# Optimization experiments

Hardware: AMD Instinct MI355X
Metric: run time of the kernel (lower is better)

Reference implementation:

```python
import jax, jax.numpy as jnp
import numpy as np

GROUPS = 8
MAX_DISP = 24
EPS = 1e-5


def group_norm(x, gamma, beta, groups):
    B, C = x.shape[0], x.shape[1]
    spatial = x.shape[2:]
    xg = x.reshape(B, groups, C // groups, -1)
    mean = xg.mean(axis=(2, 3), keepdims=True)
    var = xg.var(axis=(2, 3), keepdims=True)
    xn = ((xg - mean) * jax.lax.rsqrt(var + EPS)).reshape(B, C, *spatial)
    shp = (1, C) + (1,) * len(spatial)
    return xn * gamma.reshape(shp) + beta.reshape(shp)


def conv3d(x, w):
    return jax.lax.conv_general_dilated(x, w, (1, 1, 1), [(1, 1)] * 3,
                                        dimension_numbers=("NCDHW", "OIDHW", "NCDHW"))


def conv2d(x, w):
    return jax.lax.conv_general_dilated(x, w, (1, 1), [(1, 1)] * 2,
                                        dimension_numbers=("NCHW", "OIHW", "NCHW"))


def conv1d(x, w):
    return jax.lax.conv_general_dilated(x, w, (1,), [(1, 1)],
                                        dimension_numbers=("NCW", "OIW", "NCW"))


def setup_inputs() -> dict:
    key = jax.random.key(0)
    ks = jax.random.split(key, 12)
    B, C, H, W = 2, 64, 160, 320
    feat_out = 16
    fL = jax.random.normal(ks[0], (B, C, H, W), dtype=jnp.float32)
    fR = jax.random.normal(ks[1], (B, C, H, W), dtype=jnp.float32)
    def w(k, shape):
        fan_in = int(np.prod(shape[1:]))
        return jax.random.normal(k, shape, dtype=jnp.float32) / np.sqrt(fan_in)
    return {
        "fL": fL, "fR": fR,
        # agg: Conv3d(groups->16) GN SiLU, Conv3d(16->16) GN SiLU, Conv3d(16->1)+bias
        "agg_w1": w(ks[2], (16, GROUPS, 3, 3, 3)),
        "agg_g1": jnp.ones((16,), jnp.float32), "agg_b1": jnp.zeros((16,), jnp.float32),
        "agg_w2": w(ks[3], (16, 16, 3, 3, 3)),
        "agg_g2": jnp.ones((16,), jnp.float32), "agg_b2": jnp.zeros((16,), jnp.float32),
        "agg_w3": w(ks[4], (1, 16, 3, 3, 3)), "agg_bias3": jnp.zeros((1,), jnp.float32),
        # feat_head: Conv2d(C->feat_out) GN SiLU
        "feat_w": w(ks[5], (feat_out, C, 3, 3)),
        "feat_g": jnp.ones((feat_out,), jnp.float32), "feat_b": jnp.zeros((feat_out,), jnp.float32),
        # apc_d: Conv1d(max_disp->max_disp, k=3, no bias)
        "apc_w": w(ks[6], (MAX_DISP, MAX_DISP, 3)),
        "reg_w1": w(ks[7], (32, MAX_DISP + feat_out, 3, 3)),
        "reg_g1": jnp.ones((32,), jnp.float32), "reg_b1": jnp.zeros((32,), jnp.float32),
        "reg_w2": w(ks[8], (1, 32, 3, 3)), "reg_bias2": jnp.zeros((1,), jnp.float32),
    }


def reference(fL, fR, agg_w1, agg_g1, agg_b1, agg_w2, agg_g2, agg_b2,
              agg_w3, agg_bias3, feat_w, feat_g, feat_b, apc_w,
              reg_w1, reg_g1, reg_b1, reg_w2, reg_bias2):
    B, C, H, W = fL.shape
    G, D = GROUPS, MAX_DISP
    cg = C // G
    fL_g = fL.reshape(B, G, cg, H, W)

    # Cost volume: group-wise correlation with right feature shifted by d (zeros on left)
    def corr(d):
        fR_s = fR if d == 0 else jnp.pad(fR, ((0, 0), (0, 0), (0, 0), (d, 0)))[..., :W]
        return (fL_g * fR_s.reshape(B, G, cg, H, W)).mean(axis=2)  # [B,G,H,W]
    cv = jnp.stack([corr(d) for d in range(D)], axis=2)  # [B,G,D,H,W]

    # 3D aggregation
    h = jax.nn.silu(group_norm(conv3d(cv, agg_w1), agg_g1, agg_b1, 8))
    h = jax.nn.silu(group_norm(conv3d(h, agg_w2), agg_g2, agg_b2, 8))
    logits = (conv3d(h, agg_w3) + agg_bias3.reshape(1, 1, 1, 1, 1)).squeeze(1)  # [B,D,H,W]

    # Soft-argmin
    prob = jax.nn.softmax(logits, axis=1)
    disp_idx = jnp.arange(D, dtype=logits.dtype).reshape(1, D, 1, 1)
    d_sa = (prob * disp_idx).sum(axis=1, keepdims=True)  # [B,1,H,W]
    conf = prob.max(axis=1, keepdims=True)

    feat = jax.nn.silu(group_norm(conv2d(fL, feat_w), feat_g, feat_b, 8))  # [B,16,H,W]

    apc_out = conv1d(logits.reshape(B, D, H * W), apc_w).reshape(B, D, H, W)
    head_in = jnp.concatenate([apc_out, feat], axis=1)
    h2 = jax.nn.silu(group_norm(conv2d(head_in, reg_w1), reg_g1, reg_b1, 8))
    delta = conv2d(h2, reg_w2) + reg_bias2.reshape(1, 1, 1, 1)
    d_init = d_sa + delta

    sx = jnp.zeros_like(d_init)
    sy = jnp.zeros_like(d_init)
    return (d_init, sx, sy, feat, conf)
```

## Files before the change

### kernel.cpp

```cpp
#include <hip/hip_runtime.h>
#include <hip/hip_bf16.h>
#include <math.h>

constexpr int B_ = 2;
constexpr int C_ = 64;
constexpr int H_ = 160;
constexpr int W_ = 320;
constexpr int G_ = 8;
constexpr int D_ = 24;
constexpr int HW_ = H_ * W_;
constexpr int DHW_ = D_ * HW_;
constexpr float EPS_ = 1e-5f;

typedef __bf16 b8 __attribute__((ext_vector_type(8)));
typedef float  f4 __attribute__((ext_vector_type(4)));

__device__ inline float bf_lo(unsigned u) { return __builtin_bit_cast(float, u << 16); }
__device__ inline float bf_hi(unsigned u) { return __builtin_bit_cast(float, u & 0xffff0000u); }
__device__ inline unsigned pack2(float a, float b) {
  unsigned lo = __builtin_bit_cast(unsigned short, (__bf16)a);
  unsigned hi = __builtin_bit_cast(unsigned short, (__bf16)b);
  return (hi << 16) | lo;
}
__device__ inline float silu(float v) { return v / (1.f + __expf(-v)); }

__global__ __launch_bounds__(320)
void cv_cl_kernel(const float* __restrict__ fL, const float* __restrict__ fR,
                  __bf16* __restrict__ cv) {
  int w = threadIdx.x;
  int h = blockIdx.x % H_;
  int b = blockIdx.x / H_;
  int d0 = blockIdx.y * 6;
  const size_t rowbase = ((size_t)(b * C_) * H_ + h) * W_;
  float l[C_];
#pragma unroll
  for (int c = 0; c < C_; c++) l[c] = fL[rowbase + (size_t)c * HW_ + w];
  for (int dd = 0; dd < 6; dd++) {
    int d = d0 + dd;
    float s[8] = {0.f,0.f,0.f,0.f,0.f,0.f,0.f,0.f};
    if (w >= d) {
      const float* pr = fR + rowbase + (w - d);
#pragma unroll
      for (int c = 0; c < C_; c++) s[c >> 3] += l[c] * pr[(size_t)c * HW_];
    }
    b8 r;
#pragma unroll
    for (int g = 0; g < 8; g++) r[g] = (__bf16)(s[g] * 0.125f);
    *(b8*)(cv + ((size_t)((b * D_ + d) * H_ + h) * W_ + w) * 8) = r;
  }
}

__global__ void wprep_kernel(const float* __restrict__ w1, const float* __restrict__ w2,
                             __bf16* __restrict__ wf1, __bf16* __restrict__ wf2) {
  int lane = threadIdx.x;
  int co = lane & 15, kb = lane >> 4;
#pragma unroll
  for (int p = 0; p < 7; p++)
#pragma unroll
    for (int j = 0; j < 8; j++) {
      int kl = kb * 8 + j;
      int tap = p * 4 + (kl >> 3);
      int ci = kl & 7;
      float v = (tap <= 26) ? w1[(co * 8 + ci) * 27 + tap] : 0.f;
      wf1[(p * 64 + lane) * 8 + j] = (__bf16)v;
    }
#pragma unroll
  for (int p = 0; p < 14; p++)
#pragma unroll
    for (int j = 0; j < 8; j++) {
      int kl = kb * 8 + j;
      int tap = p * 2 + (kl >> 4);
      int ci = kl & 15;
      float v = (tap <= 26) ? w2[(co * 16 + ci) * 27 + tap] : 0.f;
      wf2[(p * 64 + lane) * 8 + j] = (__bf16)v;
    }
}

template <int CIN, int PAIRS>
__global__ __launch_bounds__(320)
void conv3d_mfma_kernel(const __bf16* __restrict__ in, const __bf16* __restrict__ wf,
                        __bf16* __restrict__ out) {
  __shared__ __align__(16) __bf16 li[9 * 162 * CIN];
  const int tid = threadIdx.x;
  int bid = blockIdx.x;
  const int wt = bid & 1; bid >>= 1;
  const int h = bid % H_;
  const int d = (bid / H_) % D_;
  const int b = bid / (H_ * D_);
  const int w0 = wt * 160;
  constexpr int VPE = CIN / 8;
  for (int idx = tid; idx < 1458 * VPE; idx += 320) {
    int entry = idx / VPE, half = idx % VPE;
    int pos = entry % 162;
    int r = entry / 162;
    int hh = r % 3, dd = r / 3;
    int dg = d + dd - 1, hg = h + hh - 1, wg = w0 + pos - 1;
    uint4 v = make_uint4(0, 0, 0, 0);
    if ((unsigned)dg < (unsigned)D_ && (unsigned)hg < (unsigned)H_ && (unsigned)wg < (unsigned)W_)
      v = *(const uint4*)(in + ((size_t)((b * D_ + dg) * H_ + hg) * W_ + wg) * CIN + half * 8);
    *(uint4*)(li + (size_t)entry * CIN + half * 8) = v;
  }
  __syncthreads();
  const int lane = tid & 63;
  const int wid = tid >> 6;
  const int m = lane & 15;
  const int tpp = 32 / CIN;
  const int tapsel = (CIN == 16) ? (lane >> 5) : (lane >> 4);
  const int ci0 = (CIN == 16) ? ((lane >> 1) & 8) : 0;
  b8 wfr[PAIRS];
#pragma unroll
  for (int p = 0; p < PAIRS; p++) wfr[p] = *(const b8*)(wf + (p * 64 + lane) * 8);
  int loff[PAIRS];
#pragma unroll
  for (int p = 0; p < PAIRS; p++) {
    int tap = p * tpp + tapsel;
    if (tap > 26) tap = 26;
    int kd = tap / 9, kh = (tap / 3) % 3, kw = tap % 3;
    loff[p] = ((kd * 3 + kh) * 162 + kw) * CIN + ci0;
  }
  const int rowbase = ((b * D_ + d) * H_ + h) * W_ + w0;
  for (int t = 0; t < 2; t++) {
    const int m0 = (wid * 2 + t) * 16;
    const int lbase = (m0 + m) * CIN;
    f4 acc = {0.f, 0.f, 0.f, 0.f};
#pragma unroll
    for (int p = 0; p < PAIRS; p++) {
      b8 a = *(const b8*)(li + lbase + loff[p]);
      acc = __builtin_amdgcn_mfma_f32_16x16x32_bf16(a, wfr[p], acc, 0, 0, 0);
    }
    const int co = lane & 15;
    const int r0 = (lane >> 4) * 4;
    const int pos0 = rowbase + m0;
#pragma unroll
    for (int r = 0; r < 4; r++)
      out[(size_t)(pos0 + r0 + r) * 16 + co] = (__bf16)acc[r];
  }
}

__global__ __launch_bounds__(256)
void stats_cl_kernel(const __bf16* __restrict__ x, double* __restrict__ st) {
  int b = blockIdx.y;
  float sg[8] = {0,0,0,0,0,0,0,0}, sq[8] = {0,0,0,0,0,0,0,0};
  for (int i = blockIdx.x * 256 + threadIdx.x; i < DHW_; i += gridDim.x * 256) {
    const uint4* p = (const uint4*)(x + ((size_t)b * DHW_ + i) * 16);
    uint4 q0 = p[0], q1 = p[1];
    unsigned us[8] = {q0.x, q0.y, q0.z, q0.w, q1.x, q1.y, q1.z, q1.w};
#pragma unroll
    for (int k = 0; k < 8; k++) {
      float v0 = bf_lo(us[k]), v1 = bf_hi(us[k]);
      sg[k] += v0 + v1;
      sq[k] += v0 * v0 + v1 * v1;
    }
  }
#pragma unroll
  for (int k = 0; k < 8; k++)
    for (int off = 32; off; off >>= 1) {
      sg[k] += __shfl_xor(sg[k], off, 64);
      sq[k] += __shfl_xor(sq[k], off, 64);
    }
  __shared__ float ls[4][16];
  int wid = threadIdx.x >> 6, lane = threadIdx.x & 63;
  if (lane == 0) {
#pragma unroll
    for (int k = 0; k < 8; k++) { ls[wid][k] = sg[k]; ls[wid][8 + k] = sq[k]; }
  }
  __syncthreads();
  if (threadIdx.x < 16) {
    float t = ls[0][threadIdx.x] + ls[1][threadIdx.x] + ls[2][threadIdx.x] + ls[3][threadIdx.x];
    int g = threadIdx.x & 7, which = threadIdx.x >> 3;
    atomicAdd(&st[(size_t)(b * 8 + g) * 2 + which], (double)t);
  }
}

__global__ __launch_bounds__(256)
void norm_cl_kernel(__bf16* __restrict__ x, const double* __restrict__ st,
                    const float* __restrict__ gamma, const float* __restrict__ beta,
                    double invN) {
  int b = blockIdx.y;
  __shared__ float scs[16], shs[16];
  if (threadIdx.x < 16) {
    int c = threadIdx.x, grp = c >> 1;
    double mean = st[(size_t)(b * 8 + grp) * 2] * invN;
    double var = st[(size_t)(b * 8 + grp) * 2 + 1] * invN - mean * mean;
    float sc = gamma[c] * rsqrtf((float)var + EPS_);
    scs[c] = sc;
    shs[c] = beta[c] - (float)mean * sc;
  }
  __syncthreads();
  float sc[16], sh[16];
#pragma unroll
  for (int c = 0; c < 16; c++) { sc[c] = scs[c]; sh[c] = shs[c]; }
  for (int i = blockIdx.x * 256 + threadIdx.x; i < DHW_; i += gridDim.x * 256) {
    uint4* p = (uint4*)(x + ((size_t)b * DHW_ + i) * 16);
    uint4 q0 = p[0], q1 = p[1];
    unsigned us[8] = {q0.x, q0.y, q0.z, q0.w, q1.x, q1.y, q1.z, q1.w};
    unsigned ro[8];
#pragma unroll
    for (int k = 0; k < 8; k++) {
      int c0 = 2 * k;
      float v0 = silu(bf_lo(us[k]) * sc[c0] + sh[c0]);
      float v1 = silu(bf_hi(us[k]) * sc[c0 + 1] + sh[c0 + 1]);
      ro[k] = pack2(v0, v1);
    }
    p[0] = make_uint4(ro[0], ro[1], ro[2], ro[3]);
    p[1] = make_uint4(ro[4], ro[5], ro[6], ro[7]);
  }
}

__global__ __launch_bounds__(256)
void conv3_tile_kernel(const __bf16* __restrict__ a2, const float* __restrict__ wt,
                       const float* __restrict__ bias, float* __restrict__ logits) {
  __shared__ __align__(16) __bf16 li[5 * 6 * 2 * 66 * 8];
  __shared__ float lw[432];
  int bid = blockIdx.x;
  int wtile = bid % 5; bid /= 5;
  int ht = bid % 40; bid /= 40;
  int dt = bid % 8; bid /= 8;
  int b = bid;
  const int d0 = dt * 3, h0 = ht * 4, w0 = wtile * 64;
  for (int i = threadIdx.x; i < 432; i += 256) {
    int tap = i >> 4, ci = i & 15;
    lw[i] = wt[ci * 27 + tap];
  }
  for (int idx = threadIdx.x; idx < 5 * 6 * 66; idx += 256) {
    int pos = idx % 66;
    int r = idx / 66;
    int hh = r % 6, dd = r / 6;
    int d = d0 + dd - 1, h = h0 + hh - 1, w = w0 + pos - 1;
    uint4 v0 = make_uint4(0, 0, 0, 0), v1 = v0;
    if ((unsigned)d < (unsigned)D_ && (unsigned)h < (unsigned)H_ && (unsigned)w < (unsigned)W_) {
      const uint4* p = (const uint4*)(a2 + ((size_t)(((b * D_ + d) * H_ + h) * W_ + w)) * 16);
      v0 = p[0];
      v1 = p[1];
    }
    int vb = ((dd * 6 + hh) * 2) * 66 + pos;
    *(uint4*)(li + (size_t)vb * 8) = v0;
    *(uint4*)(li + (size_t)(vb + 66) * 8) = v1;
  }
  __syncthreads();
  const int ow = threadIdx.x & 63;
  const int oh = threadIdx.x >> 6;
  float acc[3] = {0.f, 0.f, 0.f};
  for (int kd = 0; kd < 3; kd++)
    for (int kh = 0; kh < 3; kh++)
      for (int kw = 0; kw < 3; kw++) {
        const int tap = kd * 9 + kh * 3 + kw;
        const float* wp = lw + tap * 16;
        float wv[16];
#pragma unroll
        for (int c = 0; c < 16; c++) wv[c] = wp[c];
        const int hh = oh + kh;
        const int pos = ow + kw;
#pragma unroll
        for (int od = 0; od < 3; od++) {
          const int dd = od + kd;
          const int vb = ((dd * 6 + hh) * 2) * 66 + pos;
          uint4 q0 = *(const uint4*)(li + (size_t)vb * 8);
          uint4 q1 = *(const uint4*)(li + (size_t)(vb + 66) * 8);
          acc[od] +=
            bf_lo(q0.x) * wv[0]  + bf_hi(q0.x) * wv[1]  + bf_lo(q0.y) * wv[2]  + bf_hi(q0.y) * wv[3] +
            bf_lo(q0.z) * wv[4]  + bf_hi(q0.z) * wv[5]  + bf_lo(q0.w) * wv[6]  + bf_hi(q0.w) * wv[7] +
            bf_lo(q1.x) * wv[8]  + bf_hi(q1.x) * wv[9]  + bf_lo(q1.y) * wv[10] + bf_hi(q1.y) * wv[11] +
            bf_lo(q1.z) * wv[12] + bf_hi(q1.z) * wv[13] + bf_lo(q1.w) * wv[14] + bf_hi(q1.w) * wv[15];
        }
      }
  const float bv = bias[0];
#pragma unroll
  for (int od = 0; od < 3; od++)
    logits[((size_t)(b * D_ + d0 + od) * H_ + (h0 + oh)) * W_ + w0 + ow] = acc[od] + bv;
}

template <int C0, int C1, int COUT, int COT, bool HASBIAS, bool ADD_DSA>
__global__ __launch_bounds__(320)
void conv2d_kernel(const float* __restrict__ in0, const float* __restrict__ in1,
                   const float* __restrict__ wt, const float* __restrict__ bias,
                   const float* __restrict__ dsa, float* __restrict__ out) {
  constexpr int CINT = C0 + C1;
  constexpr int CL = COUT / COT;
  __shared__ float lw[CL * CINT * 9];
  const int co0 = blockIdx.y * CL;
  for (int i = threadIdx.x; i < CL * CINT * 9; i += 320) lw[i] = wt[co0 * CINT * 9 + i];
  __syncthreads();
  int w = threadIdx.x;
  int h = blockIdx.x % H_;
  int b = blockIdx.x / H_;
  float acc[CL];
#pragma unroll
  for (int co = 0; co < CL; co++) acc[co] = 0.f;
  for (int kh = 0; kh < 3; kh++) {
    int hh = h + kh - 1;
    if (hh < 0 || hh >= H_) continue;
    for (int kw = 0; kw < 3; kw++) {
      int ww = w + kw - 1;
      if (ww < 0 || ww >= W_) continue;
#pragma unroll
      for (int ci = 0; ci < C0; ci++) {
        float v = in0[((size_t)(b * C0 + ci)) * HW_ + hh * W_ + ww];
        const float* lwp = lw + (ci * 3 + kh) * 3 + kw;
#pragma unroll
        for (int co = 0; co < CL; co++) acc[co] += v * lwp[co * CINT * 9];
      }
      if (C1 > 0) {
#pragma unroll
        for (int ci = 0; ci < (C1 > 0 ? C1 : 1); ci++) {
          float v = in1[((size_t)(b * C1 + ci)) * HW_ + hh * W_ + ww];
          const float* lwp = lw + ((C0 + ci) * 3 + kh) * 3 + kw;
#pragma unroll
          for (int co = 0; co < CL; co++) acc[co] += v * lwp[co * CINT * 9];
        }
      }
    }
  }
#pragma unroll
  for (int co = 0; co < CL; co++) {
    float r = acc[co];
    if (HASBIAS) r += bias[co0 + co];
    if (ADD_DSA) r += dsa[(size_t)b * HW_ + h * W_ + w];
    out[((size_t)(b * COUT + co0 + co)) * HW_ + h * W_ + w] = r;
  }
}

__global__ __launch_bounds__(256)
void conv1d_kernel(const float* __restrict__ logits, const float* __restrict__ wt,
                   float* __restrict__ out) {
  __shared__ float lw[D_ * D_ * 3];
  for (int i = threadIdx.x; i < D_ * D_ * 3; i += 256) lw[i] = wt[i];
  __syncthreads();
  int idx = blockIdx.x * 256 + threadIdx.x;
  int b = idx / HW_;
  int i = idx % HW_;
  float acc[D_];
#pragma unroll
  for (int o = 0; o < D_; o++) acc[o] = 0.f;
  for (int k = 0; k < 3; k++) {
    int pos = i + k - 1;
    if (pos < 0 || pos >= HW_) continue;
#pragma unroll
    for (int din = 0; din < D_; din++) {
      float v = logits[((size_t)b * D_ + din) * HW_ + pos];
      const float* lwp = lw + din * 3 + k;
#pragma unroll
      for (int o = 0; o < D_; o++) acc[o] += v * lwp[o * D_ * 3];
    }
  }
#pragma unroll
  for (int o = 0; o < D_; o++) out[((size_t)b * D_ + o) * HW_ + i] = acc[o];
}

__global__ __launch_bounds__(256)
void stats_kernel(const float* __restrict__ x, double* __restrict__ stats,
                  int Cc, int chg, size_t per_ch, int nchunk) {
  int tmp = blockIdx.x;
  int chunk = tmp % nchunk; tmp /= nchunk;
  int cig = tmp % chg; tmp /= chg;
  int grp = tmp % 8;
  int b = tmp / 8;
  int c = grp * chg + cig;
  size_t len = per_ch / nchunk;
  const float* p = x + ((size_t)b * Cc + c) * per_ch + (size_t)chunk * len;
  float s = 0.f, s2 = 0.f;
  for (size_t i = threadIdx.x; i < len; i += 256) {
    float v = p[i];
    s += v;
    s2 += v * v;
  }
  __shared__ double ls[256], ls2[256];
  ls[threadIdx.x] = (double)s;
  ls2[threadIdx.x] = (double)s2;
  __syncthreads();
  for (int off = 128; off > 0; off >>= 1) {
    if (threadIdx.x < off) {
      ls[threadIdx.x] += ls[threadIdx.x + off];
      ls2[threadIdx.x] += ls2[threadIdx.x + off];
    }
    __syncthreads();
  }
  if (threadIdx.x == 0) {
    atomicAdd(&stats[(size_t)(b * 8 + grp) * 2], ls[0]);
    atomicAdd(&stats[(size_t)(b * 8 + grp) * 2 + 1], ls2[0]);
  }
}

__global__ __launch_bounds__(256)
void norm_silu_f32o_kernel(const float* __restrict__ x, float* __restrict__ y,
                           const double* __restrict__ stats,
                           const float* __restrict__ gamma, const float* __restrict__ beta,
                           int chg, size_t per_ch, double invN) {
  int c = blockIdx.y;
  int b = blockIdx.z;
  int grp = c / chg;
  double s = stats[(size_t)(b * 8 + grp) * 2];
  double s2 = stats[(size_t)(b * 8 + grp) * 2 + 1];
  double mean_d = s * invN;
  double var_d = s2 * invN - mean_d * mean_d;
  float sc = gamma[c] / sqrtf((float)var_d + EPS_);
  float sh = beta[c] - (float)mean_d * sc;
  size_t base = ((size_t)b * gridDim.y + c) * per_ch;
  size_t chunk = (per_ch + gridDim.x - 1) / gridDim.x;
  size_t start = (size_t)blockIdx.x * chunk;
  size_t end = start + chunk;
  if (end > per_ch) end = per_ch;
  for (size_t i = start + threadIdx.x; i < end; i += 256) {
    float v = x[base + i] * sc + sh;
    y[base + i] = v / (1.f + __expf(-v));
  }
}

__global__ __launch_bounds__(320)
void softmax_kernel(const float* __restrict__ logits, float* __restrict__ dsa,
                    float* __restrict__ conf) {
  int w = threadIdx.x;
  int h = blockIdx.x % H_;
  int b = blockIdx.x / H_;
  size_t base = ((size_t)b * D_) * HW_ + h * W_ + w;
  float v[D_];
  float m = -1e30f;
#pragma unroll
  for (int d = 0; d < D_; d++) {
    v[d] = logits[base + (size_t)d * HW_];
    m = fmaxf(m, v[d]);
  }
  float s = 0.f, wd = 0.f;
#pragma unroll
  for (int d = 0; d < D_; d++) {
    float e = __expf(v[d] - m);
    s += e;
    wd += (float)d * e;
  }
  float inv = 1.f / s;
  dsa[(size_t)b * HW_ + h * W_ + w] = wd * inv;
  conf[(size_t)b * HW_ + h * W_ + w] = inv;
}


extern "C" void kernel_launch(void* const* d_in, const int* in_sizes, int n_in,
                              void* d_out, int out_size, void* d_ws, size_t ws_size,
                              hipStream_t stream) {
  const float* fL = (const float*)d_in[0];
  const float* fR = (const float*)d_in[1];
  const float* agg_w1 = (const float*)d_in[2];
  const float* agg_g1 = (const float*)d_in[3];
  const float* agg_b1 = (const float*)d_in[4];
  const float* agg_w2 = (const float*)d_in[5];
  const float* agg_g2 = (const float*)d_in[6];
  const float* agg_b2 = (const float*)d_in[7];
  const float* agg_w3 = (const float*)d_in[8];
  const float* agg_bias3 = (const float*)d_in[9];
  const float* feat_w = (const float*)d_in[10];
  const float* feat_g = (const float*)d_in[11];
  const float* feat_b = (const float*)d_in[12];
  const float* apc_w = (const float*)d_in[13];
  const float* reg_w1 = (const float*)d_in[14];
  const float* reg_g1 = (const float*)d_in[15];
  const float* reg_b1 = (const float*)d_in[16];
  const float* reg_w2 = (const float*)d_in[17];
  const float* reg_bias2 = (const float*)d_in[18];

  char* wsb = (char*)d_ws;
  constexpr size_t REG = 78643200ull;
  __bf16* a1 = (__bf16*)wsb;
  __bf16* cvb = (__bf16*)(wsb + REG);
  __bf16* a2 = (__bf16*)(wsb + REG);
  float* logits = (float*)wsb;
  float* apc = logits + 2457600;
  float* h2 = apc + 2457600;
  float* dsa = h2 + 3276800;
  float* featraw = dsa + 102400;
  __bf16* wf1 = (__bf16*)(wsb + 2 * REG);
  __bf16* wf2 = wf1 + 3584;
  double* stats = (double*)(wsb + 2 * REG + 21504);

  float* out = (float*)d_out;
  float* out_dinit = out;
  float* out_sx = out + 102400;
  float* out_feat = out + 307200;
  float* out_conf = out + 1945600;

  hipMemsetAsync(stats, 0, 128 * sizeof(double), stream);
  hipMemsetAsync(out_sx, 0, 2 * 102400 * sizeof(float), stream);

  wprep_kernel<<<1, 64, 0, stream>>>(agg_w1, agg_w2, wf1, wf2);

  cv_cl_kernel<<<dim3(B_ * H_, 4), 320, 0, stream>>>(fL, fR, cvb);

  conv3d_mfma_kernel<8, 7><<<B_ * D_ * H_ * 2, 320, 0, stream>>>(cvb, wf1, a1);
  stats_cl_kernel<<<dim3(256, B_), 256, 0, stream>>>(a1, stats + 0);
  norm_cl_kernel<<<dim3(512, B_), 256, 0, stream>>>(a1, stats + 0, agg_g1, agg_b1,
                                                    1.0 / (2.0 * DHW_));

  conv3d_mfma_kernel<16, 14><<<B_ * D_ * H_ * 2, 320, 0, stream>>>(a1, wf2, a2);
  stats_cl_kernel<<<dim3(256, B_), 256, 0, stream>>>(a2, stats + 32);
  norm_cl_kernel<<<dim3(512, B_), 256, 0, stream>>>(a2, stats + 32, agg_g2, agg_b2,
                                                    1.0 / (2.0 * DHW_));

  conv3_tile_kernel<<<3200, 256, 0, stream>>>(a2, agg_w3, agg_bias3, logits);

  softmax_kernel<<<B_ * H_, 320, 0, stream>>>(logits, dsa, out_conf);

  conv2d_kernel<C_, 0, 16, 2, false, false><<<dim3(B_ * H_, 2), 320, 0, stream>>>(
      fL, nullptr, feat_w, nullptr, nullptr, featraw);
  stats_kernel<<<B_ * 8 * 2 * 8, 256, 0, stream>>>(featraw, stats + 64, 16, 2, (size_t)HW_, 8);
  norm_silu_f32o_kernel<<<dim3(50, 16, B_), 256, 0, stream>>>(featraw, out_feat, stats + 64,
                                                              feat_g, feat_b, 2, (size_t)HW_,
                                                              1.0 / (2.0 * HW_));

  conv1d_kernel<<<(B_ * HW_) / 256, 256, 0, stream>>>(logits, apc_w, apc);

  conv2d_kernel<D_, 16, 32, 4, false, false><<<dim3(B_ * H_, 4), 320, 0, stream>>>(
      apc, out_feat, reg_w1, nullptr, nullptr, h2);
  stats_kernel<<<B_ * 8 * 4 * 8, 256, 0, stream>>>(h2, stats + 96, 32, 4, (size_t)HW_, 8);
  norm_silu_f32o_kernel<<<dim3(50, 32, B_), 256, 0, stream>>>(h2, h2, stats + 96, reg_g1, reg_b1,
                                                              4, (size_t)HW_, 1.0 / (4.0 * HW_));

  conv2d_kernel<32, 0, 1, 1, true, true><<<dim3(B_ * H_, 1), 320, 0, stream>>>(
      h2, nullptr, reg_w2, reg_bias2, dsa, out_dinit);
}
```

Baseline: 840.5 us.

## Retile 3D conv into 3x4x64 output blocks to cut halo reloads

Each 3D conv block now computes a 3(d)x4(h)x64(w) output tile instead of a single 160-wide row. The shared-memory tile grows to a 5x6x66 halo region, and each of 4 waves loops over 12 M-tiles. Before, every output row reloaded a 3x3 halo of input rows, roughly 9x read amplification; the new tile brings that down to about 2.6x. The cost is a larger LDS footprint per block, which may reduce occupancy, and the per-block loop becomes longer.

```diff
diff --git a/kernel.cpp b/kernel.cpp
--- a/kernel.cpp
+++ b/kernel.cpp
@@ -77,24 +77,24 @@
 }
 
 template <int CIN, int PAIRS>
-__global__ __launch_bounds__(320)
+__global__ __launch_bounds__(256)
 void conv3d_mfma_kernel(const __bf16* __restrict__ in, const __bf16* __restrict__ wf,
                         __bf16* __restrict__ out) {
-  __shared__ __align__(16) __bf16 li[9 * 162 * CIN];
+  __shared__ __align__(16) __bf16 li[5 * 6 * 66 * CIN];
   const int tid = threadIdx.x;
   int bid = blockIdx.x;
-  const int wt = bid & 1; bid >>= 1;
-  const int h = bid % H_;
-  const int d = (bid / H_) % D_;
-  const int b = bid / (H_ * D_);
-  const int w0 = wt * 160;
+  int wtile = bid % 5; bid /= 5;
+  int ht = bid % 40; bid /= 40;
+  int dt = bid % 8; bid /= 8;
+  const int b = bid;
+  const int d0 = dt * 3, h0 = ht * 4, w0 = wtile * 64;
   constexpr int VPE = CIN / 8;
-  for (int idx = tid; idx < 1458 * VPE; idx += 320) {
+  for (int idx = tid; idx < 1980 * VPE; idx += 256) {
     int entry = idx / VPE, half = idx % VPE;
-    int pos = entry % 162;
-    int r = entry / 162;
-    int hh = r % 3, dd = r / 3;
-    int dg = d + dd - 1, hg = h + hh - 1, wg = w0 + pos - 1;
+    int pos = entry % 66;
+    int r = entry / 66;
+    int hh = r % 6, dd = r / 6;
+    int dg = d0 + dd - 1, hg = h0 + hh - 1, wg = w0 + pos - 1;
     uint4 v = make_uint4(0, 0, 0, 0);
     if ((unsigned)dg < (unsigned)D_ && (unsigned)hg < (unsigned)H_ && (unsigned)wg < (unsigned)W_)
       v = *(const uint4*)(in + ((size_t)((b * D_ + dg) * H_ + hg) * W_ + wg) * CIN + half * 8);
@@ -116,24 +116,27 @@
     int tap = p * tpp + tapsel;
     if (tap > 26) tap = 26;
     int kd = tap / 9, kh = (tap / 3) % 3, kw = tap % 3;
-    loff[p] = ((kd * 3 + kh) * 162 + kw) * CIN + ci0;
-  }
-  const int rowbase = ((b * D_ + d) * H_ + h) * W_ + w0;
-  for (int t = 0; t < 2; t++) {
-    const int m0 = (wid * 2 + t) * 16;
-    const int lbase = (m0 + m) * CIN;
+    loff[p] = ((kd * 6 + kh) * 66 + kw) * CIN + ci0;
+  }
+  const int co = lane & 15;
+  const int r0 = (lane >> 4) * 4;
+#pragma unroll 4
+  for (int t = 0; t < 12; t++) {
+    const int mt = wid * 12 + t;
+    const int od = mt >> 4;
+    const int rem = mt & 15;
+    const int oh = rem >> 2, wq = rem & 3;
+    const int lbase = ((od * 6 + oh) * 66 + wq * 16 + m) * CIN;
     f4 acc = {0.f, 0.f, 0.f, 0.f};
 #pragma unroll
     for (int p = 0; p < PAIRS; p++) {
       b8 a = *(const b8*)(li + lbase + loff[p]);
       acc = __builtin_amdgcn_mfma_f32_16x16x32_bf16(a, wfr[p], acc, 0, 0, 0);
     }
-    const int co = lane & 15;
-    const int r0 = (lane >> 4) * 4;
-    const int pos0 = rowbase + m0;
+    const int wbase = ((b * D_ + d0 + od) * H_ + h0 + oh) * W_ + w0 + wq * 16;
 #pragma unroll
     for (int r = 0; r < 4; r++)
-      out[(size_t)(pos0 + r0 + r) * 16 + co] = (__bf16)acc[r];
+      out[(size_t)(wbase + r0 + r) * 16 + co] = (__bf16)acc[r];
   }
 }
 
@@ -483,12 +486,12 @@
 
   cv_cl_kernel<<<dim3(B_ * H_, 4), 320, 0, stream>>>(fL, fR, cvb);
 
-  conv3d_mfma_kernel<8, 7><<<B_ * D_ * H_ * 2, 320, 0, stream>>>(cvb, wf1, a1);
+  conv3d_mfma_kernel<8, 7><<<3200, 256, 0, stream>>>(cvb, wf1, a1);
   stats_cl_kernel<<<dim3(256, B_), 256, 0, stream>>>(a1, stats + 0);
   norm_cl_kernel<<<dim3(512, B_), 256, 0, stream>>>(a1, stats + 0, agg_g1, agg_b1,
                                                     1.0 / (2.0 * DHW_));
 
-  conv3d_mfma_kernel<16, 14><<<B_ * D_ * H_ * 2, 320, 0, stream>>>(a1, wf2, a2);
+  conv3d_mfma_kernel<16, 14><<<3200, 256, 0, stream>>>(a1, wf2, a2);
   stats_cl_kernel<<<dim3(256, B_), 256, 0, stream>>>(a2, stats + 32);
   norm_cl_kernel<<<dim3(512, B_), 256, 0, stream>>>(a2, stats + 32, agg_g2, agg_b2,
                                                     1.0 / (2.0 * DHW_));
```

After: 725.2 us. 13.7% less time.
